# Kernel tuning notes

Hardware: AMD Instinct MI355X
Metric: run time of the kernel (lower is better)

## Reference

```python
import jax, jax.numpy as jnp
import numpy as np

K = 3          # neighbors for interpolation (torch_geometric default)
BIG = 1e10     # masks cross-batch pairs out of the kNN search
EPS = 1e-16    # clamp on squared distance before inverting (PyG knn_interpolate)


def setup_inputs() -> dict:
    key = jax.random.key(0)
    ks = jax.random.split(key, 8)
    N, M, C_IN, C_SKIP, H = 4096, 16384, 256, 128, 256
    x = jax.random.normal(ks[0], (N, C_IN), dtype=jnp.float32)
    pos = jax.random.normal(ks[1], (N, 3), dtype=jnp.float32)
    batch = jnp.zeros((N,), dtype=jnp.int64)
    x_skip = jax.random.normal(ks[2], (M, C_SKIP), dtype=jnp.float32)
    pos_skip = jax.random.normal(ks[3], (M, 3), dtype=jnp.float32)
    batch_skip = jnp.zeros((M,), dtype=jnp.int64)
    # MLP params: Linear(384->256) + ReLU + Linear(256->256)
    W1 = jax.random.normal(ks[4], (C_IN + C_SKIP, H), dtype=jnp.float32) * (1.0 / np.sqrt(C_IN + C_SKIP))
    b1 = jnp.zeros((H,), dtype=jnp.float32)
    W2 = jax.random.normal(ks[5], (H, H), dtype=jnp.float32) * (1.0 / np.sqrt(H))
    b2 = jnp.zeros((H,), dtype=jnp.float32)
    return {"x": x, "pos": pos, "batch": batch, "x_skip": x_skip,
            "pos_skip": pos_skip, "batch_skip": batch_skip,
            "W1": W1, "b1": b1, "W2": W2, "b2": b2}


def knn_interpolate(x, pos, pos_skip, batch, batch_skip, k):
    # squared pairwise distances [M, N] via ||q||^2 + ||p||^2 - 2 q.p (avoids [M,N,3])
    qq = jnp.sum(pos_skip * pos_skip, axis=1, keepdims=True)      # [M,1]
    pp = jnp.sum(pos * pos, axis=1)                               # [N]
    d2 = qq + pp[None, :] - 2.0 * (pos_skip @ pos.T)              # [M,N]
    d2 = d2 + jnp.where(batch_skip[:, None] != batch[None, :], BIG, 0.0)
    _, idx = jax.lax.top_k(-d2, k)                                # [M,k] nearest indices
    # recompute exact squared distances for the chosen neighbors
    nbr_pos = pos[idx]                                            # [M,k,3]
    d2k = jnp.sum((pos_skip[:, None, :] - nbr_pos) ** 2, axis=-1) # [M,k]
    w = 1.0 / jnp.clip(d2k, EPS)                                  # inverse-distance weights
    nbr_x = x[idx]                                                # [M,k,C]
    y = jnp.einsum('mk,mkc->mc', w, nbr_x) / jnp.sum(w, axis=1, keepdims=True)
    return y


def reference(x, pos, batch, x_skip, pos_skip, batch_skip, W1, b1, W2, b2):
    y = knn_interpolate(x, pos, pos_skip, batch, batch_skip, K)   # [M, C_in]
    h = jnp.concatenate([y, x_skip], axis=1)                      # [M, C_in+C_skip]
    h = jax.nn.relu(h @ W1 + b1)
    out = h @ W2 + b2
    return (out, pos_skip, batch_skip)
```

## Files before the change

kernel.cpp:

```cpp
#include <hip/hip_runtime.h>
#include <hip/hip_bf16.h>

#define N_PTS  4096
#define M_Q    16384
#define C_IN   256
#define C_SKIP 128
#define C_H    384
#define HDIM   256

typedef __bf16 bf16x8 __attribute__((ext_vector_type(8)));
typedef float  f32x4  __attribute__((ext_vector_type(4)));

__device__ __forceinline__ void insert3(float d, int j,
                                        float& b0, float& b1, float& b2,
                                        int& i0, int& i1, int& i2) {
    if (d < b2) {
        if (d < b1) {
            b2 = b1; i2 = i1;
            if (d < b0) { b1 = b0; i1 = i0; b0 = d; i0 = j; }
            else        { b1 = d;  i1 = j; }
        } else { b2 = d; i2 = j; }
    }
}

__global__ __launch_bounds__(256) void prep_tail_kernel(
        const float* __restrict__ W1, const float* __restrict__ W2,
        const float* __restrict__ pos, const float* __restrict__ pos_skip,
        __hip_bfloat16* __restrict__ W1t, __hip_bfloat16* __restrict__ W2t,
        float4* __restrict__ pos4, float* __restrict__ out, int out_size) {
    const int i = blockIdx.x * 256 + threadIdx.x;
    if (i < C_H * HDIM) {
        const int k = i / HDIM, n = i % HDIM;
        W1t[n * C_H + k] = __float2bfloat16(W1[i]);
    } else if (i < C_H * HDIM + HDIM * HDIM) {
        const int j = i - C_H * HDIM;
        const int k = j / HDIM, n = j % HDIM;
        W2t[n * HDIM + k] = __float2bfloat16(W2[j]);
    } else if (i < C_H * HDIM + HDIM * HDIM + N_PTS) {
        const int j = i - (C_H * HDIM + HDIM * HDIM);
        const float px = pos[j*3+0], py = pos[j*3+1], pz = pos[j*3+2];
        pos4[j] = make_float4(px, py, pz, px*px + py*py + pz*pz);
    }
    if (i < M_Q * 3) out[(size_t)M_Q * HDIM + i] = pos_skip[i];
    const int zbase = M_Q * HDIM + M_Q * 3;
    if (zbase + i < out_size) out[zbase + i] = 0.0f;
}

__global__ __launch_bounds__(512) void mega_kernel(
        const float4* __restrict__ pos4, const float* __restrict__ pos_skip,
        const float* __restrict__ x, const float* __restrict__ x_skip,
        const __bf16* __restrict__ W1t, const __bf16* __restrict__ W2t,
        const float* __restrict__ b1, const float* __restrict__ b2,
        float* __restrict__ out) {
    __shared__ __bf16 h[64][392];
    __shared__ __bf16 hid[64][264];
    __shared__ __bf16 Bs[256][40];
    __shared__ float candD[8][64][3];
    __shared__ int   candI[8][64][3];
    __shared__ int   idxL[192];
    __shared__ float wnL[192];

    const int t    = threadIdx.x;
    const int m0   = blockIdx.x * 64;
    const int wave = t >> 6, lane = t & 63;

    {
        const int q = m0 + lane;
        const float m2x = -2.0f * pos_skip[q*3+0];
        const float m2y = -2.0f * pos_skip[q*3+1];
        const float m2z = -2.0f * pos_skip[q*3+2];
        float bb0 = 3e38f, bb1 = 3e38f, bb2 = 3e38f;
        int   ii0 = 0, ii1 = 0, ii2 = 0;
        const int j0 = __builtin_amdgcn_readfirstlane(wave * (N_PTS / 8));
        #pragma unroll 8
        for (int j = 0; j < N_PTS / 8; ++j) {
            const float4 p = pos4[j0 + j];
            const float d = fmaf(p.x, m2x, fmaf(p.y, m2y, fmaf(p.z, m2z, p.w)));
            const int  jj = j0 + j;
            const bool c0 = d < bb0, c1 = d < bb1, c2 = d < bb2;
            ii2 = c2 ? (c1 ? ii1 : jj) : ii2;
            ii1 = c1 ? (c0 ? ii0 : jj) : ii1;
            ii0 = c0 ? jj : ii0;
            bb2 = __builtin_amdgcn_fmed3f(d, bb1, bb2);
            bb1 = __builtin_amdgcn_fmed3f(d, bb0, bb1);
            bb0 = fminf(bb0, d);
        }
        candD[wave][lane][0] = bb0; candD[wave][lane][1] = bb1; candD[wave][lane][2] = bb2;
        candI[wave][lane][0] = ii0; candI[wave][lane][1] = ii1; candI[wave][lane][2] = ii2;
    }
    __syncthreads();

    if (t < 64) {
        float B0 = 3e38f, B1 = 3e38f, B2 = 3e38f;
        int   I0 = 0, I1 = 0, I2 = 0;
        #pragma unroll
        for (int ww = 0; ww < 8; ++ww) {
            insert3(candD[ww][t][0], candI[ww][t][0], B0,B1,B2, I0,I1,I2);
            insert3(candD[ww][t][1], candI[ww][t][1], B0,B1,B2, I0,I1,I2);
            insert3(candD[ww][t][2], candI[ww][t][2], B0,B1,B2, I0,I1,I2);
        }
        const int q = m0 + t;
        const float qx = pos_skip[q*3+0], qy = pos_skip[q*3+1], qz = pos_skip[q*3+2];
        float wts[3]; const int ii[3] = {I0, I1, I2};
        #pragma unroll
        for (int r = 0; r < 3; ++r) {
            const float4 p = pos4[ii[r]];
            const float dx = qx - p.x, dy = qy - p.y, dz = qz - p.z;
            const float d2 = dx*dx + dy*dy + dz*dz;
            wts[r] = 1.0f / fmaxf(d2, 1e-16f);
        }
        const float inv = 1.0f / (wts[0] + wts[1] + wts[2]);
        idxL[t*3+0] = ii[0]; idxL[t*3+1] = ii[1]; idxL[t*3+2] = ii[2];
        wnL[t*3+0] = wts[0]*inv; wnL[t*3+1] = wts[1]*inv; wnL[t*3+2] = wts[2]*inv;
    }
    __syncthreads();

    const int brow0 = t >> 2,          bcol0 = (t & 3) * 8;
    const int brow1 = (512 + t) >> 2,  bcol1 = ((512 + t) & 3) * 8;
    int4 breg0, breg1;
    breg0 = *(const int4*)(W1t + (size_t)brow0 * C_H + bcol0);
    breg1 = *(const int4*)(W1t + (size_t)brow1 * C_H + bcol1);

    #pragma unroll 4
    for (int p = 0; p < 16; ++p) {
        const int g = p * 512 + t;
        const int r = g >> 7, c = (g & 127) * 2;
        const int   i0 = idxL[r*3+0], i1 = idxL[r*3+1], i2 = idxL[r*3+2];
        const float w0 = wnL[r*3+0],  w1 = wnL[r*3+1],  w2 = wnL[r*3+2];
        const float2 v0 = *(const float2*)(x + (size_t)i0 * C_IN + c);
        const float2 v1 = *(const float2*)(x + (size_t)i1 * C_IN + c);
        const float2 v2 = *(const float2*)(x + (size_t)i2 * C_IN + c);
        __hip_bfloat162 o;
        o.x = __float2bfloat16(w0*v0.x + w1*v1.x + w2*v2.x);
        o.y = __float2bfloat16(w0*v0.y + w1*v1.y + w2*v2.y);
        *(__hip_bfloat162*)&h[r][c] = o;
    }
    #pragma unroll 4
    for (int p = 0; p < 8; ++p) {
        const int g = p * 512 + t;
        const int r = g >> 6, c = (g & 63) * 2;
        const float2 v = *(const float2*)(x_skip + (size_t)(m0 + r) * C_SKIP + c);
        __hip_bfloat162 o;
        o.x = __float2bfloat16(v.x);
        o.y = __float2bfloat16(v.y);
        *(__hip_bfloat162*)&h[r][C_IN + c] = o;
    }

    const int ln = lane & 15, kq = lane >> 4;
    const int wm = (wave >> 2) * 32;
    const int wnc = (wave & 3) * 64;

    f32x4 acc[2][4] = {};

    for (int k0 = 0; k0 < C_H; k0 += 32) {
        __syncthreads();
        *(int4*)&Bs[brow0][bcol0] = breg0;
        *(int4*)&Bs[brow1][bcol1] = breg1;
        __syncthreads();
        if (k0 + 32 < C_H) {
            breg0 = *(const int4*)(W1t + (size_t)brow0 * C_H + (k0 + 32) + bcol0);
            breg1 = *(const int4*)(W1t + (size_t)brow1 * C_H + (k0 + 32) + bcol1);
        } else {
            breg0 = *(const int4*)(W2t + (size_t)brow0 * HDIM + bcol0);
            breg1 = *(const int4*)(W2t + (size_t)brow1 * HDIM + bcol1);
        }
        bf16x8 af[2], bfr[4];
        #pragma unroll
        for (int mt = 0; mt < 2; ++mt)
            af[mt] = *(const bf16x8*)&h[wm + mt*16 + ln][k0 + kq*8];
        #pragma unroll
        for (int nt = 0; nt < 4; ++nt)
            bfr[nt] = *(const bf16x8*)&Bs[wnc + nt*16 + ln][kq*8];
        #pragma unroll
        for (int mt = 0; mt < 2; ++mt)
            #pragma unroll
            for (int nt = 0; nt < 4; ++nt)
                acc[mt][nt] = __builtin_amdgcn_mfma_f32_16x16x32_bf16(
                                  af[mt], bfr[nt], acc[mt][nt], 0, 0, 0);
    }

    #pragma unroll
    for (int nt = 0; nt < 4; ++nt) {
        const int n = wnc + nt*16 + ln;
        const float bv = b1[n];
        #pragma unroll
        for (int mt = 0; mt < 2; ++mt) {
            const int rbase = wm + mt*16 + kq*4;
            #pragma unroll
            for (int r = 0; r < 4; ++r) {
                const float v = fmaxf(acc[mt][nt][r] + bv, 0.0f);
                hid[rbase + r][n] = (__bf16)__float2bfloat16(v);
                acc[mt][nt][r] = 0.0f;
            }
        }
    }

    for (int k0 = 0; k0 < HDIM; k0 += 32) {
        __syncthreads();
        *(int4*)&Bs[brow0][bcol0] = breg0;
        *(int4*)&Bs[brow1][bcol1] = breg1;
        __syncthreads();
        if (k0 + 32 < HDIM) {
            breg0 = *(const int4*)(W2t + (size_t)brow0 * HDIM + (k0 + 32) + bcol0);
            breg1 = *(const int4*)(W2t + (size_t)brow1 * HDIM + (k0 + 32) + bcol1);
        }
        bf16x8 af[2], bfr[4];
        #pragma unroll
        for (int mt = 0; mt < 2; ++mt)
            af[mt] = *(const bf16x8*)&hid[wm + mt*16 + ln][k0 + kq*8];
        #pragma unroll
        for (int nt = 0; nt < 4; ++nt)
            bfr[nt] = *(const bf16x8*)&Bs[wnc + nt*16 + ln][kq*8];
        #pragma unroll
        for (int mt = 0; mt < 2; ++mt)
            #pragma unroll
            for (int nt = 0; nt < 4; ++nt)
                acc[mt][nt] = __builtin_amdgcn_mfma_f32_16x16x32_bf16(
                                  af[mt], bfr[nt], acc[mt][nt], 0, 0, 0);
    }

    #pragma unroll
    for (int nt = 0; nt < 4; ++nt) {
        const int n = wnc + nt*16 + ln;
        const float bv = b2[n];
        #pragma unroll
        for (int mt = 0; mt < 2; ++mt) {
            const int rbase = m0 + wm + mt*16 + kq*4;
            #pragma unroll
            for (int r = 0; r < 4; ++r)
                out[(size_t)(rbase + r) * HDIM + n] = acc[mt][nt][r] + bv;
        }
    }
}

extern "C" void kernel_launch(void* const* d_in, const int* in_sizes, int n_in,
                              void* d_out, int out_size, void* d_ws, size_t ws_size,
                              hipStream_t stream) {
    (void)in_sizes; (void)n_in; (void)ws_size;
    const float* x        = (const float*)d_in[0];
    const float* pos      = (const float*)d_in[1];
    const float* x_skip   = (const float*)d_in[3];
    const float* pos_skip = (const float*)d_in[4];
    const float* W1       = (const float*)d_in[6];
    const float* b1       = (const float*)d_in[7];
    const float* W2       = (const float*)d_in[8];
    const float* b2       = (const float*)d_in[9];
    float* out = (float*)d_out;

    char* ws = (char*)d_ws;
    __hip_bfloat16* W1t  = (__hip_bfloat16*)(ws);
    __hip_bfloat16* W2t  = (__hip_bfloat16*)(ws + 196608);
    float4*         pos4 = (float4*)(ws + 327680);

    prep_tail_kernel<<<(C_H*HDIM + HDIM*HDIM + N_PTS + 255)/256, 256, 0, stream>>>(
        W1, W2, pos, pos_skip, W1t, W2t, pos4, out, out_size);
    mega_kernel<<<M_Q/64, 512, 0, stream>>>(
        pos4, pos_skip, x, x_skip, (const __bf16*)W1t, (const __bf16*)W2t, b1, b2, out);
}
```

Measured before the change: 147.6 us.

## Halve query block, split kNN scan into 16 slices, stream weights directly to registers

Each block now handles 32 queries instead of 64. Each wave scans two slices of the point set, so the kNN search runs over 16 slices, and the slices are merged with a cross-half shuffle. The MLP no longer stages weights through shared memory with per-k barriers: each wave owns 32 output columns and loads its W1/W2 fragments straight from global memory into registers. The neighbor weights are now computed from the expanded-form distance plus |q|^2 rather than exact recomputation, and x_skip loads are issued early to overlap the search. Each block does twice as many kNN scans per query row, and each wave reads weights from global/L2 without reuse across waves, trading block count and occupancy (launch bounds 4) for fewer barriers.

```diff
diff --git a/kernel.cpp b/kernel.cpp
--- a/kernel.cpp
+++ b/kernel.cpp
@@ -7,6 +7,7 @@
 #define C_SKIP 128
 #define C_H    384
 #define HDIM   256
+#define QBLK   32
 
 typedef __bf16 bf16x8 __attribute__((ext_vector_type(8)));
 typedef float  f32x4  __attribute__((ext_vector_type(4)));
@@ -46,35 +47,45 @@
     if (zbase + i < out_size) out[zbase + i] = 0.0f;
 }
 
-__global__ __launch_bounds__(512) void mega_kernel(
+__global__ __launch_bounds__(512, 4) void mega_kernel(
         const float4* __restrict__ pos4, const float* __restrict__ pos_skip,
         const float* __restrict__ x, const float* __restrict__ x_skip,
         const __bf16* __restrict__ W1t, const __bf16* __restrict__ W2t,
         const float* __restrict__ b1, const float* __restrict__ b2,
         float* __restrict__ out) {
-    __shared__ __bf16 h[64][392];
-    __shared__ __bf16 hid[64][264];
-    __shared__ __bf16 Bs[256][40];
-    __shared__ float candD[8][64][3];
-    __shared__ int   candI[8][64][3];
-    __shared__ int   idxL[192];
-    __shared__ float wnL[192];
+    __shared__ __bf16 h[QBLK][392];
+    __shared__ __bf16 hid[QBLK][264];
+    __shared__ float candD[16][QBLK][3];
+    __shared__ int   candI[16][QBLK][3];
+    __shared__ int   idxL[QBLK*3];
+    __shared__ float wnL[QBLK*3];
 
     const int t    = threadIdx.x;
-    const int m0   = blockIdx.x * 64;
+    const int m0   = blockIdx.x * QBLK;
     const int wave = t >> 6, lane = t & 63;
-
+    const int qh   = lane & 31;
+    const int half = lane >> 5;
+
+    float2 skipv[4];
+    #pragma unroll
+    for (int p = 0; p < 4; ++p) {
+        const int g = p * 512 + t;
+        const int r = g >> 6, c = (g & 63) * 2;
+        skipv[p] = *(const float2*)(x_skip + (size_t)(m0 + r) * C_SKIP + c);
+    }
+
+    const int q = m0 + qh;
+    const float qx = pos_skip[q*3+0], qy = pos_skip[q*3+1], qz = pos_skip[q*3+2];
+    const float m2x = -2.0f * qx, m2y = -2.0f * qy, m2z = -2.0f * qz;
     {
-        const int q = m0 + lane;
-        const float m2x = -2.0f * pos_skip[q*3+0];
-        const float m2y = -2.0f * pos_skip[q*3+1];
-        const float m2z = -2.0f * pos_skip[q*3+2];
+        const int s  = wave * 2 + half;
+        const int j0 = s * (N_PTS / 16);
         float bb0 = 3e38f, bb1 = 3e38f, bb2 = 3e38f;
         int   ii0 = 0, ii1 = 0, ii2 = 0;
-        const int j0 = __builtin_amdgcn_readfirstlane(wave * (N_PTS / 8));
+        const float4* pp = pos4 + j0;
         #pragma unroll 8
-        for (int j = 0; j < N_PTS / 8; ++j) {
-            const float4 p = pos4[j0 + j];
+        for (int j = 0; j < N_PTS / 16; ++j) {
+            const float4 p = pp[j];
             const float d = fmaf(p.x, m2x, fmaf(p.y, m2y, fmaf(p.z, m2z, p.w)));
             const int  jj = j0 + j;
             const bool c0 = d < bb0, c1 = d < bb1, c2 = d < bb2;
@@ -85,44 +96,59 @@
             bb1 = __builtin_amdgcn_fmed3f(d, bb0, bb1);
             bb0 = fminf(bb0, d);
         }
-        candD[wave][lane][0] = bb0; candD[wave][lane][1] = bb1; candD[wave][lane][2] = bb2;
-        candI[wave][lane][0] = ii0; candI[wave][lane][1] = ii1; candI[wave][lane][2] = ii2;
+        candD[s][qh][0] = bb0; candD[s][qh][1] = bb1; candD[s][qh][2] = bb2;
+        candI[s][qh][0] = ii0; candI[s][qh][1] = ii1; candI[s][qh][2] = ii2;
+    }
+    #pragma unroll
+    for (int p = 0; p < 4; ++p) {
+        const int g = p * 512 + t;
+        const int r = g >> 6, c = (g & 63) * 2;
+        __hip_bfloat162 o;
+        o.x = __float2bfloat16(skipv[p].x);
+        o.y = __float2bfloat16(skipv[p].y);
+        *(__hip_bfloat162*)&h[r][C_IN + c] = o;
     }
     __syncthreads();
 
     if (t < 64) {
-        float B0 = 3e38f, B1 = 3e38f, B2 = 3e38f;
+        const int mq = t & 31, sb = (t >> 5) * 8;
+        float B0 = 3e38f, B1 = 3e38f, B2v = 3e38f;
         int   I0 = 0, I1 = 0, I2 = 0;
         #pragma unroll
-        for (int ww = 0; ww < 8; ++ww) {
-            insert3(candD[ww][t][0], candI[ww][t][0], B0,B1,B2, I0,I1,I2);
-            insert3(candD[ww][t][1], candI[ww][t][1], B0,B1,B2, I0,I1,I2);
-            insert3(candD[ww][t][2], candI[ww][t][2], B0,B1,B2, I0,I1,I2);
-        }
-        const int q = m0 + t;
-        const float qx = pos_skip[q*3+0], qy = pos_skip[q*3+1], qz = pos_skip[q*3+2];
-        float wts[3]; const int ii[3] = {I0, I1, I2};
-        #pragma unroll
-        for (int r = 0; r < 3; ++r) {
-            const float4 p = pos4[ii[r]];
-            const float dx = qx - p.x, dy = qy - p.y, dz = qz - p.z;
-            const float d2 = dx*dx + dy*dy + dz*dz;
-            wts[r] = 1.0f / fmaxf(d2, 1e-16f);
-        }
-        const float inv = 1.0f / (wts[0] + wts[1] + wts[2]);
-        idxL[t*3+0] = ii[0]; idxL[t*3+1] = ii[1]; idxL[t*3+2] = ii[2];
-        wnL[t*3+0] = wts[0]*inv; wnL[t*3+1] = wts[1]*inv; wnL[t*3+2] = wts[2]*inv;
-    }
-    __syncthreads();
-
-    const int brow0 = t >> 2,          bcol0 = (t & 3) * 8;
-    const int brow1 = (512 + t) >> 2,  bcol1 = ((512 + t) & 3) * 8;
-    int4 breg0, breg1;
-    breg0 = *(const int4*)(W1t + (size_t)brow0 * C_H + bcol0);
-    breg1 = *(const int4*)(W1t + (size_t)brow1 * C_H + bcol1);
+        for (int s2 = 0; s2 < 8; ++s2) {
+            const int ss = sb + s2;
+            insert3(candD[ss][mq][0], candI[ss][mq][0], B0,B1,B2v, I0,I1,I2);
+            insert3(candD[ss][mq][1], candI[ss][mq][1], B0,B1,B2v, I0,I1,I2);
+            insert3(candD[ss][mq][2], candI[ss][mq][2], B0,B1,B2v, I0,I1,I2);
+        }
+        const float nb0 = __shfl_xor(B0, 32), nb1 = __shfl_xor(B1, 32), nb2 = __shfl_xor(B2v, 32);
+        const int   nI0 = __shfl_xor(I0, 32), nI1 = __shfl_xor(I1, 32), nI2 = __shfl_xor(I2, 32);
+        if (t < 32) {
+            insert3(nb0, nI0, B0,B1,B2v, I0,I1,I2);
+            insert3(nb1, nI1, B0,B1,B2v, I0,I1,I2);
+            insert3(nb2, nI2, B0,B1,B2v, I0,I1,I2);
+            const float qq = qx*qx + qy*qy + qz*qz;
+            const float w0 = 1.0f / fmaxf(B0  + qq, 1e-16f);
+            const float w1 = 1.0f / fmaxf(B1  + qq, 1e-16f);
+            const float w2 = 1.0f / fmaxf(B2v + qq, 1e-16f);
+            const float inv = 1.0f / (w0 + w1 + w2);
+            idxL[mq*3+0] = I0; idxL[mq*3+1] = I1; idxL[mq*3+2] = I2;
+            wnL[mq*3+0] = w0*inv; wnL[mq*3+1] = w1*inv; wnL[mq*3+2] = w2*inv;
+        }
+    }
+    __syncthreads();
+
+    const int ln = lane & 15, kq = lane >> 4;
+    const __bf16* w1p0 = W1t + (size_t)(wave*32 +      ln) * C_H  + kq*8;
+    const __bf16* w1p1 = W1t + (size_t)(wave*32 + 16 + ln) * C_H  + kq*8;
+    const __bf16* w2p0 = W2t + (size_t)(wave*32 +      ln) * HDIM + kq*8;
+    const __bf16* w2p1 = W2t + (size_t)(wave*32 + 16 + ln) * HDIM + kq*8;
+    bf16x8 wa0, wa1, wb0, wb1;
+    wa0 = *(const bf16x8*)(w1p0);      wa1 = *(const bf16x8*)(w1p1);
+    wb0 = *(const bf16x8*)(w1p0 + 32); wb1 = *(const bf16x8*)(w1p1 + 32);
 
     #pragma unroll 4
-    for (int p = 0; p < 16; ++p) {
+    for (int p = 0; p < 8; ++p) {
         const int g = p * 512 + t;
         const int r = g >> 7, c = (g & 127) * 2;
         const int   i0 = idxL[r*3+0], i1 = idxL[r*3+1], i2 = idxL[r*3+2];
@@ -135,57 +161,37 @@
         o.y = __float2bfloat16(w0*v0.y + w1*v1.y + w2*v2.y);
         *(__hip_bfloat162*)&h[r][c] = o;
     }
-    #pragma unroll 4
-    for (int p = 0; p < 8; ++p) {
-        const int g = p * 512 + t;
-        const int r = g >> 6, c = (g & 63) * 2;
-        const float2 v = *(const float2*)(x_skip + (size_t)(m0 + r) * C_SKIP + c);
-        __hip_bfloat162 o;
-        o.x = __float2bfloat16(v.x);
-        o.y = __float2bfloat16(v.y);
-        *(__hip_bfloat162*)&h[r][C_IN + c] = o;
-    }
-
-    const int ln = lane & 15, kq = lane >> 4;
-    const int wm = (wave >> 2) * 32;
-    const int wnc = (wave & 3) * 64;
-
-    f32x4 acc[2][4] = {};
-
-    for (int k0 = 0; k0 < C_H; k0 += 32) {
-        __syncthreads();
-        *(int4*)&Bs[brow0][bcol0] = breg0;
-        *(int4*)&Bs[brow1][bcol1] = breg1;
-        __syncthreads();
-        if (k0 + 32 < C_H) {
-            breg0 = *(const int4*)(W1t + (size_t)brow0 * C_H + (k0 + 32) + bcol0);
-            breg1 = *(const int4*)(W1t + (size_t)brow1 * C_H + (k0 + 32) + bcol1);
-        } else {
-            breg0 = *(const int4*)(W2t + (size_t)brow0 * HDIM + bcol0);
-            breg1 = *(const int4*)(W2t + (size_t)brow1 * HDIM + bcol1);
-        }
-        bf16x8 af[2], bfr[4];
-        #pragma unroll
-        for (int mt = 0; mt < 2; ++mt)
-            af[mt] = *(const bf16x8*)&h[wm + mt*16 + ln][k0 + kq*8];
-        #pragma unroll
-        for (int nt = 0; nt < 4; ++nt)
-            bfr[nt] = *(const bf16x8*)&Bs[wnc + nt*16 + ln][kq*8];
-        #pragma unroll
-        for (int mt = 0; mt < 2; ++mt)
-            #pragma unroll
-            for (int nt = 0; nt < 4; ++nt)
-                acc[mt][nt] = __builtin_amdgcn_mfma_f32_16x16x32_bf16(
-                                  af[mt], bfr[nt], acc[mt][nt], 0, 0, 0);
-    }
-
-    #pragma unroll
-    for (int nt = 0; nt < 4; ++nt) {
-        const int n = wnc + nt*16 + ln;
+    __syncthreads();
+
+    f32x4 acc[2][2] = {};
+
+    #pragma unroll
+    for (int k0 = 0; k0 < C_H; k0 += 64) {
+        bf16x8 af0 = *(const bf16x8*)&h[     ln][k0 + kq*8];
+        bf16x8 af1 = *(const bf16x8*)&h[16 + ln][k0 + kq*8];
+        acc[0][0] = __builtin_amdgcn_mfma_f32_16x16x32_bf16(af0, wa0, acc[0][0], 0,0,0);
+        acc[0][1] = __builtin_amdgcn_mfma_f32_16x16x32_bf16(af0, wa1, acc[0][1], 0,0,0);
+        acc[1][0] = __builtin_amdgcn_mfma_f32_16x16x32_bf16(af1, wa0, acc[1][0], 0,0,0);
+        acc[1][1] = __builtin_amdgcn_mfma_f32_16x16x32_bf16(af1, wa1, acc[1][1], 0,0,0);
+        if (k0 + 64 < C_H) { wa0 = *(const bf16x8*)(w1p0 + k0+64); wa1 = *(const bf16x8*)(w1p1 + k0+64); }
+        else               { wa0 = *(const bf16x8*)(w2p0);         wa1 = *(const bf16x8*)(w2p1); }
+        bf16x8 bf0 = *(const bf16x8*)&h[     ln][k0+32 + kq*8];
+        bf16x8 bf1 = *(const bf16x8*)&h[16 + ln][k0+32 + kq*8];
+        acc[0][0] = __builtin_amdgcn_mfma_f32_16x16x32_bf16(bf0, wb0, acc[0][0], 0,0,0);
+        acc[0][1] = __builtin_amdgcn_mfma_f32_16x16x32_bf16(bf0, wb1, acc[0][1], 0,0,0);
+        acc[1][0] = __builtin_amdgcn_mfma_f32_16x16x32_bf16(bf1, wb0, acc[1][0], 0,0,0);
+        acc[1][1] = __builtin_amdgcn_mfma_f32_16x16x32_bf16(bf1, wb1, acc[1][1], 0,0,0);
+        if (k0 + 96 < C_H) { wb0 = *(const bf16x8*)(w1p0 + k0+96); wb1 = *(const bf16x8*)(w1p1 + k0+96); }
+        else               { wb0 = *(const bf16x8*)(w2p0 + (k0+96-C_H)); wb1 = *(const bf16x8*)(w2p1 + (k0+96-C_H)); }
+    }
+
+    #pragma unroll
+    for (int nt = 0; nt < 2; ++nt) {
+        const int n = wave*32 + nt*16 + ln;
         const float bv = b1[n];
         #pragma unroll
         for (int mt = 0; mt < 2; ++mt) {
-            const int rbase = wm + mt*16 + kq*4;
+            const int rbase = mt*16 + kq*4;
             #pragma unroll
             for (int r = 0; r < 4; ++r) {
                 const float v = fmaxf(acc[mt][nt][r] + bv, 0.0f);
@@ -194,38 +200,33 @@
             }
         }
     }
-
-    for (int k0 = 0; k0 < HDIM; k0 += 32) {
-        __syncthreads();
-        *(int4*)&Bs[brow0][bcol0] = breg0;
-        *(int4*)&Bs[brow1][bcol1] = breg1;
-        __syncthreads();
-        if (k0 + 32 < HDIM) {
-            breg0 = *(const int4*)(W2t + (size_t)brow0 * HDIM + (k0 + 32) + bcol0);
-            breg1 = *(const int4*)(W2t + (size_t)brow1 * HDIM + (k0 + 32) + bcol1);
-        }
-        bf16x8 af[2], bfr[4];
-        #pragma unroll
-        for (int mt = 0; mt < 2; ++mt)
-            af[mt] = *(const bf16x8*)&hid[wm + mt*16 + ln][k0 + kq*8];
-        #pragma unroll
-        for (int nt = 0; nt < 4; ++nt)
-            bfr[nt] = *(const bf16x8*)&Bs[wnc + nt*16 + ln][kq*8];
-        #pragma unroll
-        for (int mt = 0; mt < 2; ++mt)
-            #pragma unroll
-            for (int nt = 0; nt < 4; ++nt)
-                acc[mt][nt] = __builtin_amdgcn_mfma_f32_16x16x32_bf16(
-                                  af[mt], bfr[nt], acc[mt][nt], 0, 0, 0);
-    }
-
-    #pragma unroll
-    for (int nt = 0; nt < 4; ++nt) {
-        const int n = wnc + nt*16 + ln;
+    __syncthreads();
+
+    #pragma unroll
+    for (int k0 = 0; k0 < HDIM; k0 += 64) {
+        bf16x8 af0 = *(const bf16x8*)&hid[     ln][k0 + kq*8];
+        bf16x8 af1 = *(const bf16x8*)&hid[16 + ln][k0 + kq*8];
+        acc[0][0] = __builtin_amdgcn_mfma_f32_16x16x32_bf16(af0, wa0, acc[0][0], 0,0,0);
+        acc[0][1] = __builtin_amdgcn_mfma_f32_16x16x32_bf16(af0, wa1, acc[0][1], 0,0,0);
+        acc[1][0] = __builtin_amdgcn_mfma_f32_16x16x32_bf16(af1, wa0, acc[1][0], 0,0,0);
+        acc[1][1] = __builtin_amdgcn_mfma_f32_16x16x32_bf16(af1, wa1, acc[1][1], 0,0,0);
+        if (k0 + 64 < HDIM) { wa0 = *(const bf16x8*)(w2p0 + k0+64); wa1 = *(const bf16x8*)(w2p1 + k0+64); }
+        bf16x8 bf0 = *(const bf16x8*)&hid[     ln][k0+32 + kq*8];
+        bf16x8 bf1 = *(const bf16x8*)&hid[16 + ln][k0+32 + kq*8];
+        acc[0][0] = __builtin_amdgcn_mfma_f32_16x16x32_bf16(bf0, wb0, acc[0][0], 0,0,0);
+        acc[0][1] = __builtin_amdgcn_mfma_f32_16x16x32_bf16(bf0, wb1, acc[0][1], 0,0,0);
+        acc[1][0] = __builtin_amdgcn_mfma_f32_16x16x32_bf16(bf1, wb0, acc[1][0], 0,0,0);
+        acc[1][1] = __builtin_amdgcn_mfma_f32_16x16x32_bf16(bf1, wb1, acc[1][1], 0,0,0);
+        if (k0 + 96 < HDIM) { wb0 = *(const bf16x8*)(w2p0 + k0+96); wb1 = *(const bf16x8*)(w2p1 + k0+96); }
+    }
+
+    #pragma unroll
+    for (int nt = 0; nt < 2; ++nt) {
+        const int n = wave*32 + nt*16 + ln;
         const float bv = b2[n];
         #pragma unroll
         for (int mt = 0; mt < 2; ++mt) {
-            const int rbase = m0 + wm + mt*16 + kq*4;
+            const int rbase = m0 + mt*16 + kq*4;
             #pragma unroll
             for (int r = 0; r < 4; ++r)
                 out[(size_t)(rbase + r) * HDIM + n] = acc[mt][nt][r] + bv;
@@ -254,6 +255,6 @@
 
     prep_tail_kernel<<<(C_H*HDIM + HDIM*HDIM + N_PTS + 255)/256, 256, 0, stream>>>(
         W1, W2, pos, pos_skip, W1t, W2t, pos4, out, out_size);
-    mega_kernel<<<M_Q/64, 512, 0, stream>>>(
+    mega_kernel<<<M_Q/QBLK, 512, 0, stream>>>(
         pos4, pos_skip, x, x_skip, (const __bf16*)W1t, (const __bf16*)W2t, b1, b2, out);
 }
```

After: 143.0 us. -3.1%, faster.

## Stage point positions in LDS and stream MFMA weight fragments from global

Applied to the files above, without the earlier changes.

Copies all point positions into shared memory before the kNN scan so the per-query loop reads LDS instead of global memory. Replaces the shared B-tile staging with per-wave register double-buffered weight fragments loaded directly from global, removing two block barriers per K step. Weights are derived from the kNN expanded distance instead of being recomputed exactly, and gathers are widened to float4 with shared memory aliased across phases. This raises LDS use to about 100KB and can lose accuracy when distances are tiny.

```diff
diff --git a/kernel.cpp b/kernel.cpp
--- a/kernel.cpp
+++ b/kernel.cpp
@@ -7,6 +7,7 @@
 #define C_SKIP 128
 #define C_H    384
 #define HDIM   256
+#define QB     64
 
 typedef __bf16 bf16x8 __attribute__((ext_vector_type(8)));
 typedef float  f32x4  __attribute__((ext_vector_type(4)));
@@ -52,29 +53,43 @@
         const __bf16* __restrict__ W1t, const __bf16* __restrict__ W2t,
         const float* __restrict__ b1, const float* __restrict__ b2,
         float* __restrict__ out) {
-    __shared__ __bf16 h[64][392];
-    __shared__ __bf16 hid[64][264];
-    __shared__ __bf16 Bs[256][40];
-    __shared__ float candD[8][64][3];
-    __shared__ int   candI[8][64][3];
-    __shared__ int   idxL[192];
-    __shared__ float wnL[192];
+    __shared__ __align__(16) char smem[100864];
+    float4*         posL  = (float4*)smem;
+    __hip_bfloat16* h     = (__hip_bfloat16*)smem;
+    __hip_bfloat16* hid   = (__hip_bfloat16*)(smem + 65536);
+    float*          candD = (float*)(smem + 65536);
+    int*            candI = (int*)  (smem + 71680);
+    int*            idxL  = (int*)  (smem + 99328);
+    float*          wnL   = (float*)(smem + 100096);
 
     const int t    = threadIdx.x;
-    const int m0   = blockIdx.x * 64;
+    const int m0   = blockIdx.x * QB;
     const int wave = t >> 6, lane = t & 63;
 
+    #pragma unroll
+    for (int k = 0; k < N_PTS / 512; ++k)
+        posL[k * 512 + t] = pos4[k * 512 + t];
+
+    float4 skipv[4];
+    #pragma unroll
+    for (int p = 0; p < 4; ++p) {
+        const int g = p * 512 + t;
+        const int r = g >> 5, c = (g & 31) * 4;
+        skipv[p] = *(const float4*)(x_skip + (size_t)(m0 + r) * C_SKIP + c);
+    }
+
+    const int q = m0 + lane;
+    const float qx = pos_skip[q*3+0], qy = pos_skip[q*3+1], qz = pos_skip[q*3+2];
+    const float m2x = -2.0f * qx, m2y = -2.0f * qy, m2z = -2.0f * qz;
+    __syncthreads();
+
     {
-        const int q = m0 + lane;
-        const float m2x = -2.0f * pos_skip[q*3+0];
-        const float m2y = -2.0f * pos_skip[q*3+1];
-        const float m2z = -2.0f * pos_skip[q*3+2];
+        const int j0 = wave * (N_PTS / 8);
         float bb0 = 3e38f, bb1 = 3e38f, bb2 = 3e38f;
         int   ii0 = 0, ii1 = 0, ii2 = 0;
-        const int j0 = __builtin_amdgcn_readfirstlane(wave * (N_PTS / 8));
         #pragma unroll 8
         for (int j = 0; j < N_PTS / 8; ++j) {
-            const float4 p = pos4[j0 + j];
+            const float4 p = posL[j0 + j];
             const float d = fmaf(p.x, m2x, fmaf(p.y, m2y, fmaf(p.z, m2z, p.w)));
             const int  jj = j0 + j;
             const bool c0 = d < bb0, c1 = d < bb1, c2 = d < bb2;
@@ -85,98 +100,93 @@
             bb1 = __builtin_amdgcn_fmed3f(d, bb0, bb1);
             bb0 = fminf(bb0, d);
         }
-        candD[wave][lane][0] = bb0; candD[wave][lane][1] = bb1; candD[wave][lane][2] = bb2;
-        candI[wave][lane][0] = ii0; candI[wave][lane][1] = ii1; candI[wave][lane][2] = ii2;
+        const int ci = (wave * 64 + lane) * 3;
+        candD[ci+0] = bb0; candD[ci+1] = bb1; candD[ci+2] = bb2;
+        candI[ci+0] = ii0; candI[ci+1] = ii1; candI[ci+2] = ii2;
     }
     __syncthreads();
 
     if (t < 64) {
-        float B0 = 3e38f, B1 = 3e38f, B2 = 3e38f;
+        float B0 = 3e38f, B1 = 3e38f, B2v = 3e38f;
         int   I0 = 0, I1 = 0, I2 = 0;
         #pragma unroll
         for (int ww = 0; ww < 8; ++ww) {
-            insert3(candD[ww][t][0], candI[ww][t][0], B0,B1,B2, I0,I1,I2);
-            insert3(candD[ww][t][1], candI[ww][t][1], B0,B1,B2, I0,I1,I2);
-            insert3(candD[ww][t][2], candI[ww][t][2], B0,B1,B2, I0,I1,I2);
-        }
-        const int q = m0 + t;
-        const float qx = pos_skip[q*3+0], qy = pos_skip[q*3+1], qz = pos_skip[q*3+2];
-        float wts[3]; const int ii[3] = {I0, I1, I2};
-        #pragma unroll
-        for (int r = 0; r < 3; ++r) {
-            const float4 p = pos4[ii[r]];
-            const float dx = qx - p.x, dy = qy - p.y, dz = qz - p.z;
-            const float d2 = dx*dx + dy*dy + dz*dz;
-            wts[r] = 1.0f / fmaxf(d2, 1e-16f);
-        }
-        const float inv = 1.0f / (wts[0] + wts[1] + wts[2]);
-        idxL[t*3+0] = ii[0]; idxL[t*3+1] = ii[1]; idxL[t*3+2] = ii[2];
-        wnL[t*3+0] = wts[0]*inv; wnL[t*3+1] = wts[1]*inv; wnL[t*3+2] = wts[2]*inv;
-    }
-    __syncthreads();
-
-    const int brow0 = t >> 2,          bcol0 = (t & 3) * 8;
-    const int brow1 = (512 + t) >> 2,  bcol1 = ((512 + t) & 3) * 8;
-    int4 breg0, breg1;
-    breg0 = *(const int4*)(W1t + (size_t)brow0 * C_H + bcol0);
-    breg1 = *(const int4*)(W1t + (size_t)brow1 * C_H + bcol1);
-
-    #pragma unroll 4
-    for (int p = 0; p < 16; ++p) {
+            const int ci = (ww * 64 + t) * 3;
+            insert3(candD[ci+0], candI[ci+0], B0,B1,B2v, I0,I1,I2);
+            insert3(candD[ci+1], candI[ci+1], B0,B1,B2v, I0,I1,I2);
+            insert3(candD[ci+2], candI[ci+2], B0,B1,B2v, I0,I1,I2);
+        }
+        const float qq = qx*qx + qy*qy + qz*qz;
+        const float w0 = 1.0f / fmaxf(B0  + qq, 1e-16f);
+        const float w1 = 1.0f / fmaxf(B1  + qq, 1e-16f);
+        const float w2 = 1.0f / fmaxf(B2v + qq, 1e-16f);
+        const float inv = 1.0f / (w0 + w1 + w2);
+        idxL[t*3+0] = I0; idxL[t*3+1] = I1; idxL[t*3+2] = I2;
+        wnL[t*3+0] = w0*inv; wnL[t*3+1] = w1*inv; wnL[t*3+2] = w2*inv;
+    }
+    __syncthreads();
+
+    const int ln = lane & 15, kq = lane >> 4;
+    const int wm  = (wave >> 2) * 32;
+    const int wnc = (wave & 3) * 64;
+
+    bf16x8 bfA[4], bfB[4];
+    #pragma unroll
+    for (int nt = 0; nt < 4; ++nt) {
+        bfA[nt] = *(const bf16x8*)(W1t + (size_t)(wnc + nt*16 + ln) * C_H +  0 + kq*8);
+        bfB[nt] = *(const bf16x8*)(W1t + (size_t)(wnc + nt*16 + ln) * C_H + 32 + kq*8);
+    }
+
+    #pragma unroll
+    for (int p = 0; p < 4; ++p) {
         const int g = p * 512 + t;
-        const int r = g >> 7, c = (g & 127) * 2;
-        const int   i0 = idxL[r*3+0], i1 = idxL[r*3+1], i2 = idxL[r*3+2];
-        const float w0 = wnL[r*3+0],  w1 = wnL[r*3+1],  w2 = wnL[r*3+2];
-        const float2 v0 = *(const float2*)(x + (size_t)i0 * C_IN + c);
-        const float2 v1 = *(const float2*)(x + (size_t)i1 * C_IN + c);
-        const float2 v2 = *(const float2*)(x + (size_t)i2 * C_IN + c);
-        __hip_bfloat162 o;
-        o.x = __float2bfloat16(w0*v0.x + w1*v1.x + w2*v2.x);
-        o.y = __float2bfloat16(w0*v0.y + w1*v1.y + w2*v2.y);
-        *(__hip_bfloat162*)&h[r][c] = o;
+        const int r = g >> 5, c = (g & 31) * 4;
+        union { __hip_bfloat162 v2[2]; uint2 u; } pk;
+        pk.v2[0].x = __float2bfloat16(skipv[p].x); pk.v2[0].y = __float2bfloat16(skipv[p].y);
+        pk.v2[1].x = __float2bfloat16(skipv[p].z); pk.v2[1].y = __float2bfloat16(skipv[p].w);
+        *(uint2*)&h[(size_t)r * 392 + C_IN + c] = pk.u;
     }
     #pragma unroll 4
     for (int p = 0; p < 8; ++p) {
         const int g = p * 512 + t;
-        const int r = g >> 6, c = (g & 63) * 2;
-        const float2 v = *(const float2*)(x_skip + (size_t)(m0 + r) * C_SKIP + c);
-        __hip_bfloat162 o;
-        o.x = __float2bfloat16(v.x);
-        o.y = __float2bfloat16(v.y);
-        *(__hip_bfloat162*)&h[r][C_IN + c] = o;
-    }
-
-    const int ln = lane & 15, kq = lane >> 4;
-    const int wm = (wave >> 2) * 32;
-    const int wnc = (wave & 3) * 64;
+        const int r = g >> 6, c = (g & 63) * 4;
+        const int   i0 = idxL[r*3+0], i1 = idxL[r*3+1], i2 = idxL[r*3+2];
+        const float w0 = wnL[r*3+0],  w1 = wnL[r*3+1],  w2 = wnL[r*3+2];
+        const float4 v0 = *(const float4*)(x + (size_t)i0 * C_IN + c);
+        const float4 v1 = *(const float4*)(x + (size_t)i1 * C_IN + c);
+        const float4 v2 = *(const float4*)(x + (size_t)i2 * C_IN + c);
+        union { __hip_bfloat162 v2_[2]; uint2 u; } pk;
+        pk.v2_[0].x = __float2bfloat16(w0*v0.x + w1*v1.x + w2*v2.x);
+        pk.v2_[0].y = __float2bfloat16(w0*v0.y + w1*v1.y + w2*v2.y);
+        pk.v2_[1].x = __float2bfloat16(w0*v0.z + w1*v1.z + w2*v2.z);
+        pk.v2_[1].y = __float2bfloat16(w0*v0.w + w1*v1.w + w2*v2.w);
+        *(uint2*)&h[(size_t)r * 392 + c] = pk.u;
+    }
+    __syncthreads();
 
     f32x4 acc[2][4] = {};
 
-    for (int k0 = 0; k0 < C_H; k0 += 32) {
-        __syncthreads();
-        *(int4*)&Bs[brow0][bcol0] = breg0;
-        *(int4*)&Bs[brow1][bcol1] = breg1;
-        __syncthreads();
-        if (k0 + 32 < C_H) {
-            breg0 = *(const int4*)(W1t + (size_t)brow0 * C_H + (k0 + 32) + bcol0);
-            breg1 = *(const int4*)(W1t + (size_t)brow1 * C_H + (k0 + 32) + bcol1);
+    #pragma unroll
+    for (int s = 0; s < 12; ++s) {
+        const int k0 = s * 32;
+        bf16x8* bc = (s & 1) ? bfB : bfA;
+        const bf16x8 a0 = *(const bf16x8*)&h[(size_t)(wm +      ln) * 392 + k0 + kq*8];
+        const bf16x8 a1 = *(const bf16x8*)&h[(size_t)(wm + 16 + ln) * 392 + k0 + kq*8];
+        #pragma unroll
+        for (int nt = 0; nt < 4; ++nt)
+            acc[0][nt] = __builtin_amdgcn_mfma_f32_16x16x32_bf16(a0, bc[nt], acc[0][nt], 0,0,0);
+        #pragma unroll
+        for (int nt = 0; nt < 4; ++nt)
+            acc[1][nt] = __builtin_amdgcn_mfma_f32_16x16x32_bf16(a1, bc[nt], acc[1][nt], 0,0,0);
+        if (s < 10) {
+            #pragma unroll
+            for (int nt = 0; nt < 4; ++nt)
+                bc[nt] = *(const bf16x8*)(W1t + (size_t)(wnc + nt*16 + ln) * C_H + (k0 + 64) + kq*8);
         } else {
-            breg0 = *(const int4*)(W2t + (size_t)brow0 * HDIM + bcol0);
-            breg1 = *(const int4*)(W2t + (size_t)brow1 * HDIM + bcol1);
-        }
-        bf16x8 af[2], bfr[4];
-        #pragma unroll
-        for (int mt = 0; mt < 2; ++mt)
-            af[mt] = *(const bf16x8*)&h[wm + mt*16 + ln][k0 + kq*8];
-        #pragma unroll
-        for (int nt = 0; nt < 4; ++nt)
-            bfr[nt] = *(const bf16x8*)&Bs[wnc + nt*16 + ln][kq*8];
-        #pragma unroll
-        for (int mt = 0; mt < 2; ++mt)
             #pragma unroll
             for (int nt = 0; nt < 4; ++nt)
-                acc[mt][nt] = __builtin_amdgcn_mfma_f32_16x16x32_bf16(
-                                  af[mt], bfr[nt], acc[mt][nt], 0, 0, 0);
+                bc[nt] = *(const bf16x8*)(W2t + (size_t)(wnc + nt*16 + ln) * HDIM + (s - 10) * 32 + kq*8);
+        }
     }
 
     #pragma unroll
@@ -189,34 +199,30 @@
             #pragma unroll
             for (int r = 0; r < 4; ++r) {
                 const float v = fmaxf(acc[mt][nt][r] + bv, 0.0f);
-                hid[rbase + r][n] = (__bf16)__float2bfloat16(v);
+                hid[(size_t)(rbase + r) * 264 + n] = __float2bfloat16(v);
                 acc[mt][nt][r] = 0.0f;
             }
         }
     }
-
-    for (int k0 = 0; k0 < HDIM; k0 += 32) {
-        __syncthreads();
-        *(int4*)&Bs[brow0][bcol0] = breg0;
-        *(int4*)&Bs[brow1][bcol1] = breg1;
-        __syncthreads();
-        if (k0 + 32 < HDIM) {
-            breg0 = *(const int4*)(W2t + (size_t)brow0 * HDIM + (k0 + 32) + bcol0);
-            breg1 = *(const int4*)(W2t + (size_t)brow1 * HDIM + (k0 + 32) + bcol1);
-        }
-        bf16x8 af[2], bfr[4];
-        #pragma unroll
-        for (int mt = 0; mt < 2; ++mt)
-            af[mt] = *(const bf16x8*)&hid[wm + mt*16 + ln][k0 + kq*8];
-        #pragma unroll
-        for (int nt = 0; nt < 4; ++nt)
-            bfr[nt] = *(const bf16x8*)&Bs[wnc + nt*16 + ln][kq*8];
-        #pragma unroll
-        for (int mt = 0; mt < 2; ++mt)
+    __syncthreads();
+
+    #pragma unroll
+    for (int s = 0; s < 8; ++s) {
+        const int k0 = s * 32;
+        bf16x8* bc = (s & 1) ? bfB : bfA;
+        const bf16x8 a0 = *(const bf16x8*)&hid[(size_t)(wm +      ln) * 264 + k0 + kq*8];
+        const bf16x8 a1 = *(const bf16x8*)&hid[(size_t)(wm + 16 + ln) * 264 + k0 + kq*8];
+        #pragma unroll
+        for (int nt = 0; nt < 4; ++nt)
+            acc[0][nt] = __builtin_amdgcn_mfma_f32_16x16x32_bf16(a0, bc[nt], acc[0][nt], 0,0,0);
+        #pragma unroll
+        for (int nt = 0; nt < 4; ++nt)
+            acc[1][nt] = __builtin_amdgcn_mfma_f32_16x16x32_bf16(a1, bc[nt], acc[1][nt], 0,0,0);
+        if (s < 6) {
             #pragma unroll
             for (int nt = 0; nt < 4; ++nt)
-                acc[mt][nt] = __builtin_amdgcn_mfma_f32_16x16x32_bf16(
-                                  af[mt], bfr[nt], acc[mt][nt], 0, 0, 0);
+                bc[nt] = *(const bf16x8*)(W2t + (size_t)(wnc + nt*16 + ln) * HDIM + (k0 + 64) + kq*8);
+        }
     }
 
     #pragma unroll
@@ -254,6 +260,6 @@
 
     prep_tail_kernel<<<(C_H*HDIM + HDIM*HDIM + N_PTS + 255)/256, 256, 0, stream>>>(
         W1, W2, pos, pos_skip, W1t, W2t, pos4, out, out_size);
-    mega_kernel<<<M_Q/64, 512, 0, stream>>>(
+    mega_kernel<<<M_Q/QB, 512, 0, stream>>>(
         pos4, pos_skip, x, x_skip, (const __bf16*)W1t, (const __bf16*)W2t, b1, b2, out);
 }
```

Result: faster. 140.4 us (-4.9%).
